# Performance work log

Hardware: AMD Instinct MI355X
Metric: run time of the kernel (lower is better)

## Reference

```python
import jax, jax.numpy as jnp
import numpy as np

DIM = 1024
NUM_HEADS = 16
HEAD_DIM = DIM // NUM_HEADS
EPS = 1e-6


def setup_inputs() -> dict:
    key = jax.random.key(0)
    ks = jax.random.split(key, 9)
    B, N = 4, 4096
    scale = 1.0 / np.sqrt(DIM)
    inp = {
        "query": jax.random.normal(ks[0], (B, N, DIM), dtype=jnp.float32),
        "Wq": jax.random.normal(ks[1], (DIM, DIM), dtype=jnp.float32) * scale,
        "bq": jnp.zeros((DIM,), dtype=jnp.float32),
        "Wk": jax.random.normal(ks[2], (DIM, DIM), dtype=jnp.float32) * scale,
        "bk": jnp.zeros((DIM,), dtype=jnp.float32),
        "Wv": jax.random.normal(ks[3], (DIM, DIM), dtype=jnp.float32) * scale,
        "bv": jnp.zeros((DIM,), dtype=jnp.float32),
        "Wo": jax.random.normal(ks[4], (DIM, DIM), dtype=jnp.float32) * scale,
        "bo": jnp.zeros((DIM,), dtype=jnp.float32),
    }
    return inp


def _feature_map(x):
    # elu(x) + 1
    return jax.nn.elu(x) + 1.0


def reference(query, Wq, bq, Wk, bk, Wv, bv, Wo, bo):
    B, N, C = query.shape
    H, D = NUM_HEADS, HEAD_DIM
    # projections (torch Linear: x @ W.T + b)
    q = (query @ Wq.T + bq).reshape(B, N, H, D).transpose(0, 2, 1, 3)  # bhnd
    k = (query @ Wk.T + bk).reshape(B, N, H, D).transpose(0, 2, 1, 3)  # bhsd
    v = (query @ Wv.T + bv).reshape(B, N, H, D).transpose(0, 2, 1, 3)  # bhse
    q = _feature_map(q)
    k = _feature_map(k)
    # kv aggregation: [B,H,D,D]
    kv = jnp.einsum('bhsd,bhse->bhde', k, v)
    attn = jnp.einsum('bhqd,bhde->bhqe', q, kv)
    k_sum = k.sum(axis=2)  # bhd
    normalizer = jnp.einsum('bhqd,bhd->bhq', q, k_sum)[..., None] + EPS
    attn = attn / normalizer
    attn = attn.transpose(0, 2, 1, 3).reshape(B, N, C)
    # dropout p=0 -> identity
    return attn @ Wo.T + bo
```

## Files before the change

kernel.cpp:

```cpp
#include <hip/hip_runtime.h>

typedef __attribute__((ext_vector_type(8))) short short8;
typedef __attribute__((ext_vector_type(4))) float f32x4;

#define DEV static __device__ __forceinline__

DEV float bf2f(unsigned short b) { return __uint_as_float(((unsigned)b) << 16); }
DEV unsigned short f2bf(float f) {
  unsigned u = __float_as_uint(f);
  u += 0x7FFFu + ((u >> 16) & 1u);
  return (unsigned short)(u >> 16);
}

__global__ __launch_bounds__(256) void cast_bf16(const float* __restrict__ src,
                                                 unsigned short* __restrict__ dst, int n4) {
  int i = blockIdx.x * 256 + threadIdx.x;
  if (i >= n4) return;
  float4 f = ((const float4*)src)[i];
  unsigned lo = (unsigned)f2bf(f.x) | ((unsigned)f2bf(f.y) << 16);
  unsigned hi = (unsigned)f2bf(f.z) | ((unsigned)f2bf(f.w) << 16);
  ((uint2*)dst)[i] = make_uint2(lo, hi);
}

__global__ __launch_bounds__(256) void cast_w4(
    const float* __restrict__ w0, const float* __restrict__ w1,
    const float* __restrict__ w2, const float* __restrict__ w3,
    unsigned short* __restrict__ o0, unsigned short* __restrict__ o1,
    unsigned short* __restrict__ o2, unsigned short* __restrict__ o3) {
  const int which = blockIdx.y;
  const float* s = (which == 0) ? w0 : (which == 1) ? w1 : (which == 2) ? w2 : w3;
  unsigned short* d = (which == 0) ? o0 : (which == 1) ? o1 : (which == 2) ? o2 : o3;
  const int i = blockIdx.x * 256 + threadIdx.x;
  float4 f = ((const float4*)s)[i];
  unsigned lo = (unsigned)f2bf(f.x) | ((unsigned)f2bf(f.y) << 16);
  unsigned hi = (unsigned)f2bf(f.z) | ((unsigned)f2bf(f.w) << 16);
  ((uint2*)d)[i] = make_uint2(lo, hi);
}


DEV void stage_half(const unsigned short* __restrict__ g, int row0, int ldk, int kcol,
                    unsigned short* lbuf, int half, int wave, int lane) {
#pragma unroll
  for (int j = 0; j < 2; ++j) {
    const int row_lin = half * 128 + j * 64 + wave * 8 + (lane >> 3);
    const int k_src = (((lane & 7) ^ ((lane >> 3) & 7)) * 8);
    const unsigned short* src = g + (size_t)(row0 + row_lin) * ldk + kcol + k_src;
    unsigned short* dst = lbuf + half * 8192 + j * 4096 + wave * 512;
    __builtin_amdgcn_global_load_lds((const __attribute__((address_space(1))) void*)src,
                                     (__attribute__((address_space(3))) void*)dst, 16, 0, 0);
  }
}

#define BAR() do { asm volatile("" ::: "memory"); __builtin_amdgcn_s_barrier(); \
                   asm volatile("" ::: "memory"); } while (0)
#define VMC(n) asm volatile("s_waitcnt vmcnt(" #n ")" ::: "memory")

#define READ_Aset(dst, qr, base) \
  _Pragma("unroll") for (int i4 = 0; i4 < 4; ++i4) \
  _Pragma("unroll") for (int ks = 0; ks < 2; ++ks) { \
    const int r_ = wrow + (qr) * 64 + i4 * 16 + fr; \
    dst[i4][ks] = *(const short8*)((base) + r_ * 128 + ((ks * 64 + kq16) ^ flip)); }

#define READ_Bset(dst, qc, base) \
  _Pragma("unroll") for (int c2 = 0; c2 < 2; ++c2) \
  _Pragma("unroll") for (int ks = 0; ks < 2; ++ks) { \
    const int c_ = wcol + (qc) * 32 + c2 * 16 + fr; \
    dst[c2][ks] = *(const short8*)((base) + c_ * 128 + ((ks * 64 + kq16) ^ flip)); }

#define MMQ(qr, qc, A_, B_) \
  _Pragma("unroll") for (int i4 = 0; i4 < 4; ++i4) \
  _Pragma("unroll") for (int c2 = 0; c2 < 2; ++c2) \
  _Pragma("unroll") for (int ks = 0; ks < 2; ++ks) \
    acc[(qr) * 4 + i4][(qc) * 2 + c2] = __builtin_amdgcn_mfma_f32_16x16x32_bf16( \
        A_[i4][ks], B_[c2][ks], acc[(qr) * 4 + i4][(qc) * 2 + c2], 0, 0, 0);

template<int EPI>
__global__ __launch_bounds__(512, 2) void gemm256(
    const unsigned short* __restrict__ A, const unsigned short* __restrict__ Bt,
    const float* __restrict__ bias0, const float* __restrict__ bias1,
    const float* __restrict__ bias2,
    float* __restrict__ outF,
    unsigned short* __restrict__ oQ, unsigned short* __restrict__ oK,
    unsigned short* __restrict__ oV,
    int M, int N, int K)
{
  __shared__ alignas(16) unsigned short As[2][16384];
  __shared__ alignas(16) unsigned short Bs[2][16384];
  const int tid  = threadIdx.x;
  const int lane = tid & 63;
  const int wave = tid >> 6;
  const int wr = wave >> 2, wc = wave & 3;
  const int fr   = lane & 15;
  const int kq16 = (lane >> 4) * 16;
  const int flip = (fr & 7) << 4;
  const int nwg = gridDim.x, cpx = nwg >> 3, orig = blockIdx.x;
  const int logical = (orig & 7) * cpx + (orig >> 3);
  const int ntc = N >> 8;
  const int brow = (logical / ntc) << 8;
  const int bcol = (logical % ntc) << 8;
  const int NT = K >> 6;
  const int wrow = wr * 128, wcol = wc * 64;

  f32x4 acc[8][4] = {};
  short8 a[4][2], b0[2][2], b1[2][2];

  stage_half(A,  brow, K, 0, &As[0][0], 0, wave, lane);
  stage_half(A,  brow, K, 0, &As[0][0], 1, wave, lane);
  stage_half(Bt, bcol, K, 0, &Bs[0][0], 0, wave, lane);
  stage_half(Bt, bcol, K, 0, &Bs[0][0], 1, wave, lane);
  VMC(0);
  BAR();

  for (int t = 0; t < NT; ++t) {
    const int cur = t & 1;
    const char* Ac = (const char*)&As[cur][0];
    const char* Bc = (const char*)&Bs[cur][0];
    const int k1 = (t + 1) << 6;
    const bool hasN1 = t < NT - 1;

    if (hasN1) {
      stage_half(A,  brow, K, k1, &As[cur ^ 1][0], 0, wave, lane);
      stage_half(A,  brow, K, k1, &As[cur ^ 1][0], 1, wave, lane);
      stage_half(Bt, bcol, K, k1, &Bs[cur ^ 1][0], 0, wave, lane);
      stage_half(Bt, bcol, K, k1, &Bs[cur ^ 1][0], 1, wave, lane);
    }

    READ_Aset(a, 0, Ac)
    READ_Bset(b0, 0, Bc)
    READ_Bset(b1, 1, Bc)
    __builtin_amdgcn_s_setprio(1);
    MMQ(0, 0, a, b0)
    MMQ(0, 1, a, b1)
    __builtin_amdgcn_s_setprio(0);
    READ_Aset(a, 1, Ac)
    __builtin_amdgcn_s_setprio(1);
    MMQ(1, 0, a, b0)
    MMQ(1, 1, a, b1)
    __builtin_amdgcn_s_setprio(0);

    VMC(0);
    BAR();
  }

  const int l4 = (lane >> 4) * 4;
#pragma unroll
  for (int rg = 0; rg < 8; ++rg) {
    const int row0 = brow + wrow + rg * 16 + l4;
#pragma unroll
    for (int cg = 0; cg < 4; ++cg) {
      const int col = bcol + wcol + cg * 16 + fr;
      if (EPI == 1) {
        const float bb = bias0[col];
#pragma unroll
        for (int q = 0; q < 4; ++q)
          outF[(size_t)(row0 + q) * N + col] = acc[rg][cg][q] + bb;
      } else {
        const int sel = col >> 10;
        const int o = col & 1023;
        const float* bp = (sel == 0) ? bias0 : (sel == 1) ? bias1 : bias2;
        unsigned short* dstp = (sel == 0) ? oQ : (sel == 1) ? oK : oV;
        const float bb = bp[o];
        const int h = o >> 6, d = o & 63;
#pragma unroll
        for (int q = 0; q < 4; ++q) {
          const int rr = row0 + q;
          const int bi = rr >> 12, n = rr & 4095;
          float val = acc[rg][cg][q] + bb;
          if (sel < 2) val = (val > 0.f) ? (val + 1.f) : __expf(val);
          dstp[((size_t)((bi * 16 + h) * 4096 + n)) * 64 + d] = f2bf(val);
        }
      }
    }
  }
}

__global__ __launch_bounds__(256) void kv_agg(
    const unsigned short* __restrict__ kbuf, const unsigned short* __restrict__ vbuf,
    float* __restrict__ part_kv, float* __restrict__ part_ks)
{
  __shared__ alignas(16) unsigned short Ksm[16 * 64];
  __shared__ alignas(16) unsigned short Vsm[16 * 64];
  const int blk = blockIdx.x;
  const int bh = blk >> 4, chunk = blk & 15;
  const int t = threadIdx.x;
  const int d0 = (t >> 4) * 4;
  const int e0 = (t & 15) * 4;
  float acc[4][4] = {};
  float ks[4] = {0.f, 0.f, 0.f, 0.f};
  const size_t base = ((size_t)bh * 4096 + chunk * 256) * 64;
  for (int ss = 0; ss < 256; ss += 16) {
    __syncthreads();
    if (t < 128) *(uint4*)&Ksm[t * 8] = *(const uint4*)&kbuf[base + (size_t)ss * 64 + t * 8];
    else         *(uint4*)&Vsm[(t - 128) * 8] = *(const uint4*)&vbuf[base + (size_t)ss * 64 + (t - 128) * 8];
    __syncthreads();
#pragma unroll
    for (int i = 0; i < 16; ++i) {
      const unsigned ku0 = *(const unsigned*)&Ksm[i * 64 + d0];
      const unsigned ku1 = *(const unsigned*)&Ksm[i * 64 + d0 + 2];
      const unsigned vu0 = *(const unsigned*)&Vsm[i * 64 + e0];
      const unsigned vu1 = *(const unsigned*)&Vsm[i * 64 + e0 + 2];
      const float kk0 = __uint_as_float(ku0 << 16), kk1 = __uint_as_float(ku0 & 0xFFFF0000u);
      const float kk2 = __uint_as_float(ku1 << 16), kk3 = __uint_as_float(ku1 & 0xFFFF0000u);
      const float vv0 = __uint_as_float(vu0 << 16), vv1 = __uint_as_float(vu0 & 0xFFFF0000u);
      const float vv2 = __uint_as_float(vu1 << 16), vv3 = __uint_as_float(vu1 & 0xFFFF0000u);
      ks[0] += kk0; ks[1] += kk1; ks[2] += kk2; ks[3] += kk3;
      acc[0][0] += kk0 * vv0; acc[0][1] += kk0 * vv1; acc[0][2] += kk0 * vv2; acc[0][3] += kk0 * vv3;
      acc[1][0] += kk1 * vv0; acc[1][1] += kk1 * vv1; acc[1][2] += kk1 * vv2; acc[1][3] += kk1 * vv3;
      acc[2][0] += kk2 * vv0; acc[2][1] += kk2 * vv1; acc[2][2] += kk2 * vv2; acc[2][3] += kk2 * vv3;
      acc[3][0] += kk3 * vv0; acc[3][1] += kk3 * vv1; acc[3][2] += kk3 * vv2; acc[3][3] += kk3 * vv3;
    }
  }
#pragma unroll
  for (int r = 0; r < 4; ++r)
    *(float4*)&part_kv[((size_t)blk * 64 + d0 + r) * 64 + e0] =
        make_float4(acc[r][0], acc[r][1], acc[r][2], acc[r][3]);
  if ((t & 15) == 0) {
#pragma unroll
    for (int r = 0; r < 4; ++r) part_ks[blk * 64 + d0 + r] = ks[r];
  }
}

__global__ __launch_bounds__(256) void kv_reduce(
    const float* __restrict__ part_kv, const float* __restrict__ part_ks,
    float* __restrict__ kvf, float* __restrict__ ksf)
{
  const int bh = blockIdx.x;
  const int t = threadIdx.x;
#pragma unroll
  for (int i = 0; i < 16; ++i) {
    const int lin = i * 256 + t;
    float s = 0.f;
#pragma unroll
    for (int c = 0; c < 16; ++c) s += part_kv[((size_t)(bh * 16 + c)) * 4096 + lin];
    kvf[(size_t)bh * 4096 + lin] = s;
  }
  if (t < 64) {
    float s = 0.f;
#pragma unroll
    for (int c = 0; c < 16; ++c) s += part_ks[(bh * 16 + c) * 64 + t];
    ksf[bh * 64 + t] = s;
  }
}

__global__ __launch_bounds__(256) void attn_norm(
    const unsigned short* __restrict__ qbuf, const float* __restrict__ kvf,
    const float* __restrict__ ksf, unsigned short* __restrict__ attnb)
{
  __shared__ alignas(16) float kv_lds[4096];
  __shared__ alignas(16) float ks_lds[64];
  __shared__ alignas(16) unsigned short q_lds[4096];
  const int blk = blockIdx.x;
  const int bh = blk >> 6, nt = blk & 63;
  const int b = bh >> 4, h = bh & 15;
  const int t = threadIdx.x;
#pragma unroll
  for (int i = 0; i < 4; ++i) {
    const int lin = i * 1024 + t * 4;
    *(float4*)&kv_lds[lin] = *(const float4*)&kvf[(size_t)bh * 4096 + lin];
  }
  if (t < 64) ks_lds[t] = ksf[bh * 64 + t];
  const size_t qbase = ((size_t)bh * 4096 + nt * 64) * 64;
#pragma unroll
  for (int r = 0; r < 2; ++r)
    *(uint4*)&q_lds[(r * 256 + t) * 8] = *(const uint4*)&qbuf[qbase + (r * 256 + t) * 8];
  __syncthreads();

  const int n_loc = t >> 2, e0 = (t & 3) * 16;
  float num[16] = {};
  float den = 0.f;
  for (int d = 0; d < 64; ++d) {
    const float qd = bf2f(q_lds[n_loc * 64 + d]);
    den += qd * ks_lds[d];
    const float* kvp = &kv_lds[d * 64 + e0];
#pragma unroll
    for (int j = 0; j < 16; ++j) num[j] += qd * kvp[j];
  }
  const float inv = 1.f / (den + 1e-6f);
  unsigned uo[8];
#pragma unroll
  for (int p = 0; p < 8; ++p) {
    const unsigned short a0 = f2bf(num[2 * p] * inv);
    const unsigned short a1 = f2bf(num[2 * p + 1] * inv);
    uo[p] = (unsigned)a0 | ((unsigned)a1 << 16);
  }
  const size_t obase = ((size_t)(b * 4096 + nt * 64 + n_loc)) * 1024 + h * 64 + e0;
  *(uint4*)&attnb[obase]     = make_uint4(uo[0], uo[1], uo[2], uo[3]);
  *(uint4*)&attnb[obase + 8] = make_uint4(uo[4], uo[5], uo[6], uo[7]);
}

extern "C" void kernel_launch(void* const* d_in, const int* in_sizes, int n_in,
                              void* d_out, int out_size, void* d_ws, size_t ws_size,
                              hipStream_t stream)
{
  const float* query = (const float*)d_in[0];
  const float* Wq = (const float*)d_in[1];
  const float* bq = (const float*)d_in[2];
  const float* Wk = (const float*)d_in[3];
  const float* bk = (const float*)d_in[4];
  const float* Wv = (const float*)d_in[5];
  const float* bv = (const float*)d_in[6];
  const float* Wo = (const float*)d_in[7];
  const float* bo = (const float*)d_in[8];
  float* out = (float*)d_out;

  const int M = in_sizes[0] / 1024;

  char* ws = (char*)d_ws;
  unsigned short* qbf   = (unsigned short*)(ws);
  unsigned short* attnb = (unsigned short*)(ws);
  unsigned short* wqkv  = (unsigned short*)(ws + 33554432);
  unsigned short* wobf  = (unsigned short*)(ws + 39845888);
  unsigned short* phiq  = (unsigned short*)(ws + 41943040);
  unsigned short* phik  = (unsigned short*)(ws + 75497472);
  unsigned short* vbf   = (unsigned short*)(ws + 109051904);
  float*          pkv   = (float*)(ws + 142606336);
  float*          pks   = (float*)(ws + 159383552);
  float*          kvf   = (float*)(ws + 159645696);
  float*          ksf   = (float*)(ws + 160694272);

  cast_bf16<<<(M * 1024 / 4 + 255) / 256, 256, 0, stream>>>(query, qbf, M * 1024 / 4);
  cast_w4<<<dim3(1024, 4), 256, 0, stream>>>(Wq, Wk, Wv, Wo,
                                             wqkv, wqkv + 1048576, wqkv + 2097152, wobf);

  gemm256<0><<<dim3((M / 256) * (3072 / 256)), 512, 0, stream>>>(
      qbf, wqkv, bq, bk, bv, nullptr, phiq, phik, vbf, M, 3072, 1024);

  kv_agg<<<1024, 256, 0, stream>>>(phik, vbf, pkv, pks);

  kv_reduce<<<64, 256, 0, stream>>>(pkv, pks, kvf, ksf);

  attn_norm<<<4096, 256, 0, stream>>>(phiq, kvf, ksf, attnb);

  gemm256<1><<<dim3((M / 256) * (1024 / 256)), 512, 0, stream>>>(
      attnb, wobf, bo, nullptr, nullptr, out, nullptr, nullptr, nullptr, M, 1024, 1024);
}
```

Before: 275.3 us.

## Restructure GEMM main loop into 8-wave ping-pong schedule with staggered half-tile prefetch

Replaces the simple double-buffered K loop with an unrolled-by-two schedule. Each tile is split into four MFMA phases separated by barriers and explicit lgkmcnt waits, and half-tile global-to-LDS loads for tiles t+1 and t+2 are interleaved between phases. The goal is to overlap global loads with MFMA work and avoid draining vmcnt to zero every iteration. It adds many more barriers per tile, and the partial-vmcnt bookkeeping (VMC(6)) must exactly match the number of loads in flight. The loop also assumes NT is even, which holds for K=1024.

```diff
diff --git a/kernel.cpp b/kernel.cpp
--- a/kernel.cpp
+++ b/kernel.cpp
@@ -53,6 +53,7 @@
 
 #define BAR() do { asm volatile("" ::: "memory"); __builtin_amdgcn_s_barrier(); \
                    asm volatile("" ::: "memory"); } while (0)
+#define LGKM0() asm volatile("s_waitcnt lgkmcnt(0)" ::: "memory")
 #define VMC(n) asm volatile("s_waitcnt vmcnt(" #n ")" ::: "memory")
 
 #define READ_Aset(dst, qr, base) \
@@ -73,6 +74,40 @@
   _Pragma("unroll") for (int ks = 0; ks < 2; ++ks) \
     acc[(qr) * 4 + i4][(qc) * 2 + c2] = __builtin_amdgcn_mfma_f32_16x16x32_bf16( \
         A_[i4][ks], B_[c2][ks], acc[(qr) * 4 + i4][(qc) * 2 + c2], 0, 0, 0);
+
+#define TILE_BODY(tt, CURBUF, NXTBUF) do { \
+  const char* Ac = (const char*)&As[CURBUF][0]; \
+  const char* Bc = (const char*)&Bs[CURBUF][0]; \
+  const int t_ = (tt); \
+  const bool h1 = (t_ + 1 < NT), h2 = (t_ + 2 < NT); \
+  const int k1 = (t_ + 1) << 6, k2 = (t_ + 2) << 6; \
+   \
+  if (h1) stage_half(A, brow, K, k1, &As[NXTBUF][0], 1, wave, lane); \
+  READ_Aset(a, 0, Ac) \
+  READ_Bset(b0, 0, Bc) \
+  BAR(); LGKM0(); \
+  __builtin_amdgcn_s_setprio(1); MMQ(0, 0, a, b0) __builtin_amdgcn_s_setprio(0); \
+  BAR(); \
+   \
+  READ_Bset(b1, 1, Bc) \
+  BAR(); LGKM0(); \
+  __builtin_amdgcn_s_setprio(1); MMQ(0, 1, a, b1) __builtin_amdgcn_s_setprio(0); \
+  BAR(); \
+   \
+  if (h2) stage_half(Bt, bcol, K, k2, &Bs[CURBUF][0], 0, wave, lane); \
+  READ_Aset(a, 1, Ac) \
+  BAR(); LGKM0(); \
+  __builtin_amdgcn_s_setprio(1); MMQ(1, 0, a, b0) __builtin_amdgcn_s_setprio(0); \
+  BAR(); \
+   \
+  if (h2) { stage_half(Bt, bcol, K, k2, &Bs[CURBUF][0], 1, wave, lane); \
+            stage_half(A,  brow, K, k2, &As[CURBUF][0], 0, wave, lane); } \
+  BAR(); \
+  __builtin_amdgcn_s_setprio(1); MMQ(1, 1, a, b1) __builtin_amdgcn_s_setprio(0); \
+  if (h2)      { VMC(6); } \
+  else if (h1) { VMC(0); } \
+  BAR(); \
+} while (0)
 
 template<int EPI>
 __global__ __launch_bounds__(512, 2) void gemm256(
@@ -108,38 +143,15 @@
   stage_half(A,  brow, K, 0, &As[0][0], 1, wave, lane);
   stage_half(Bt, bcol, K, 0, &Bs[0][0], 0, wave, lane);
   stage_half(Bt, bcol, K, 0, &Bs[0][0], 1, wave, lane);
-  VMC(0);
+  stage_half(Bt, bcol, K, 64, &Bs[1][0], 0, wave, lane);
+  stage_half(Bt, bcol, K, 64, &Bs[1][0], 1, wave, lane);
+  stage_half(A,  brow, K, 64, &As[1][0], 0, wave, lane);
+  VMC(6);
   BAR();
 
-  for (int t = 0; t < NT; ++t) {
-    const int cur = t & 1;
-    const char* Ac = (const char*)&As[cur][0];
-    const char* Bc = (const char*)&Bs[cur][0];
-    const int k1 = (t + 1) << 6;
-    const bool hasN1 = t < NT - 1;
-
-    if (hasN1) {
-      stage_half(A,  brow, K, k1, &As[cur ^ 1][0], 0, wave, lane);
-      stage_half(A,  brow, K, k1, &As[cur ^ 1][0], 1, wave, lane);
-      stage_half(Bt, bcol, K, k1, &Bs[cur ^ 1][0], 0, wave, lane);
-      stage_half(Bt, bcol, K, k1, &Bs[cur ^ 1][0], 1, wave, lane);
-    }
-
-    READ_Aset(a, 0, Ac)
-    READ_Bset(b0, 0, Bc)
-    READ_Bset(b1, 1, Bc)
-    __builtin_amdgcn_s_setprio(1);
-    MMQ(0, 0, a, b0)
-    MMQ(0, 1, a, b1)
-    __builtin_amdgcn_s_setprio(0);
-    READ_Aset(a, 1, Ac)
-    __builtin_amdgcn_s_setprio(1);
-    MMQ(1, 0, a, b0)
-    MMQ(1, 1, a, b1)
-    __builtin_amdgcn_s_setprio(0);
-
-    VMC(0);
-    BAR();
+  for (int t = 0; t < NT; t += 2) {
+    TILE_BODY(t,     0, 1);
+    TILE_BODY(t + 1, 1, 0);
   }
 
   const int l4 = (lane >> 4) * 4;
```

Result: no change. 279.3 us (+1.4%).
